# Kernel tuning notes

Hardware: AMD Instinct MI355X
Metric: run time of the kernel (lower is better)

Reference implementation:

```python
import jax, jax.numpy as jnp
import numpy as np

INPUT_SIZE = 64
HIDDEN = 256
BATCH = 128
SEQ = 1000


def setup_inputs() -> dict:
    key = jax.random.key(0)
    ks = jax.random.split(key, 17)
    s_in = 1.0 / np.sqrt(INPUT_SIZE)
    s_h = 1.0 / np.sqrt(HIDDEN)
    d = {"x": jax.random.normal(ks[0], (BATCH, SEQ, INPUT_SIZE), dtype=jnp.float32)}
    names_ih = ["W_ii", "W_if", "W_ig", "W_io"]
    names_hh = ["W_hi", "W_hf", "W_hg", "W_ho"]
    for i, n in enumerate(names_ih):
        d[n] = jax.random.uniform(ks[1 + i], (HIDDEN, INPUT_SIZE), minval=-s_in, maxval=s_in, dtype=jnp.float32)
        d["b" + n[1:]] = jax.random.uniform(ks[5 + i], (HIDDEN,), minval=-s_in, maxval=s_in, dtype=jnp.float32)
    for i, n in enumerate(names_hh):
        d[n] = jax.random.uniform(ks[9 + i], (HIDDEN, HIDDEN), minval=-s_h, maxval=s_h, dtype=jnp.float32)
        d["b" + n[1:]] = jax.random.uniform(ks[13 + i], (HIDDEN,), minval=-s_h, maxval=s_h, dtype=jnp.float32)
    return d


def _lstm(x, W_ii, b_ii, W_if, b_if, W_ig, b_ig, W_io, b_io,
          W_hi, b_hi, W_hf, b_hf, W_hg, b_hg, W_ho, b_ho):
    B = x.shape[0]
    H = W_ii.shape[0]
    # Precompute all input-to-hidden projections for every timestep in one
    # batched GEMM per gate (the recurrence only needs the h-to-h part).
    # Shapes: [B, T, H] each; then move time to the leading axis for scan.
    xi = jnp.einsum('bti,hi->tbh', x, W_ii) + b_ii
    xf = jnp.einsum('bti,hi->tbh', x, W_if) + b_if
    xg = jnp.einsum('bti,hi->tbh', x, W_ig) + b_ig
    xo = jnp.einsum('bti,hi->tbh', x, W_io) + b_io

    h0 = jnp.zeros((B, H), dtype=x.dtype)
    c0 = jnp.zeros((B, H), dtype=x.dtype)

    def step(carry, xs):
        h, c = carry
        xi_t, xf_t, xg_t, xo_t = xs
        i_t = jax.nn.sigmoid(xi_t + h @ W_hi.T + b_hi)
        f_t = jax.nn.sigmoid(xf_t + h @ W_hf.T + b_hf)
        g_t = jnp.tanh(xg_t + h @ W_hg.T + b_hg)
        o_t = jax.nn.sigmoid(xo_t + h @ W_ho.T + b_ho)
        c_new = f_t * c + i_t * g_t
        h_new = o_t * jnp.tanh(c_new)
        return (h_new, c_new), h_new

    (h_n, c_n), out_tbh = jax.lax.scan(step, (h0, c0), (xi, xf, xg, xo))
    output = jnp.transpose(out_tbh, (1, 0, 2))  # [B, T, H]
    return output, h_n[None], c_n[None]


def reference(x, W_ii, b_ii, W_if, b_if, W_ig, b_ig, W_io, b_io,
              W_hi, b_hi, W_hf, b_hf, W_hg, b_hg, W_ho, b_ho):
    return _lstm(x, W_ii, b_ii, W_if, b_if, W_ig, b_ig, W_io, b_io,
                 W_hi, b_hi, W_hf, b_hf, W_hg, b_hg, W_ho, b_ho)
```

## Files before the change

### kernel.cpp

```cpp
#include <hip/hip_runtime.h>

#define INPUT 64
#define HID 256
#define BATCH 128
#define TSTEPS 1000
#define KTOT 320

typedef __bf16 bf16_t;
typedef __bf16 bf16x8 __attribute__((ext_vector_type(8)));
typedef float  f32x4  __attribute__((ext_vector_type(4)));

#define WPACK_OFF   0
#define WPACK_BYTES (1024 * KTOT * 2)
#define BIAS_OFF    (WPACK_OFF + WPACK_BYTES)
#define BIAS_BYTES  (1024 * 4)
#define EXCH_OFF    (BIAS_OFF + BIAS_BYTES)
#define EXCH_BYTES  (16 * 2 * 2048 * 2)
#define FLAG_OFF    (EXCH_OFF + EXCH_BYTES)

__global__ void lstm_prep(
    const float* __restrict__ Wii, const float* __restrict__ Wif,
    const float* __restrict__ Wig, const float* __restrict__ Wio,
    const float* __restrict__ Whi, const float* __restrict__ Whf,
    const float* __restrict__ Whg, const float* __restrict__ Who,
    const float* __restrict__ bii, const float* __restrict__ bif,
    const float* __restrict__ big, const float* __restrict__ bio,
    const float* __restrict__ bhi, const float* __restrict__ bhf,
    const float* __restrict__ bhg, const float* __restrict__ bho,
    bf16_t* __restrict__ wpack, float* __restrict__ bias,
    int* __restrict__ flags)
{
    int id = blockIdx.x * 256 + threadIdx.x;
    if (id < 1024 * KTOT) {
        int n = id / KTOT, k = id % KTOT;
        int g = n >> 8, j = n & 255;
        const float* Wh = (g == 0) ? Whi : (g == 1) ? Whf : (g == 2) ? Whg : Who;
        const float* Wi = (g == 0) ? Wii : (g == 1) ? Wif : (g == 2) ? Wig : Wio;
        float v = (k < HID) ? Wh[j * HID + k] : Wi[j * INPUT + (k - HID)];
        wpack[id] = (bf16_t)v;
    }
    if (id < 1024) {
        int g = id >> 8, j = id & 255;
        const float* bi = (g == 0) ? bii : (g == 1) ? bif : (g == 2) ? big : bio;
        const float* bh = (g == 0) ? bhi : (g == 1) ? bhf : (g == 2) ? bhg : bho;
        bias[id] = bi[j] + bh[j];
    }
    if (id < 16)
        __hip_atomic_store(flags + id * 64, 0, __ATOMIC_RELAXED, __HIP_MEMORY_SCOPE_AGENT);
}

__device__ __forceinline__ float sigmoid_f(float v) {
    return 1.0f / (1.0f + __expf(-v));
}
__device__ __forceinline__ float tanh_f(float v) {
    return 1.0f - 2.0f / (__expf(2.0f * v) + 1.0f);
}

__global__ __launch_bounds__(512) void lstm_main(
    const float* __restrict__ x, const bf16_t* __restrict__ wpack,
    const float* __restrict__ bias_g, float* __restrict__ out,
    bf16_t* __restrict__ exch, int* __restrict__ flags)
{
    __shared__ __align__(16) bf16_t hxx[2][16 * 328];

    const int bid   = blockIdx.x;
    const int group = bid & 7;
    const int half  = bid >> 3;
    const int tid   = threadIdx.x;
    const int w     = tid >> 6;
    const int l     = tid & 63;
    const int col   = l & 15;
    const int kb    = l >> 4;

    const int jloc  = w * 16 + col;
    const int jglob = half * 128 + jloc;

    bf16x8 bW[4][10];
#pragma unroll
    for (int g = 0; g < 4; ++g) {
        const bf16_t* wrow = wpack + (size_t)(g * 256 + jglob) * KTOT;
#pragma unroll
        for (int ks = 0; ks < 10; ++ks)
            bW[g][ks] = *(const bf16x8*)(wrow + ks * 32 + kb * 8);
    }
#pragma unroll
    for (int g = 0; g < 4; ++g)
#pragma unroll
        for (int ks = 0; ks < 10; ++ks)
            asm volatile("" : "+v"(bW[g][ks]));

    float bias_r[4];
#pragma unroll
    for (int g = 0; g < 4; ++g)
        bias_r[g] = bias_g[g * 256 + jglob];

    float c_st[4] = {0.f, 0.f, 0.f, 0.f};

    const int pbid = (1 - half) * 8 + group;
    int*       flag_me = flags + bid * 64;
    const int* flag_pn = flags + pbid * 64;
    const int  pbase   = (1 - half) * 128;

    const int xb = tid >> 5;
    const int xi = (tid & 31) * 2;
    const float* xbase = x + (size_t)(group * 16 + xb) * (TSTEPS * INPUT) + xi;

    const int prow = tid >> 5;
    const int pe0  = (tid & 31) * 4;

    {
        float2 v = *(const float2*)(xbase);
        hxx[0][xb * 328 + 256 + xi]     = (bf16_t)v.x;
        hxx[0][xb * 328 + 256 + xi + 1] = (bf16_t)v.y;
    }
    float2 xv = *(const float2*)(xbase + INPUT);
    __syncthreads();

#pragma unroll 1
    for (int t = 0; t < TSTEPS; ++t) {
        const int cur = t & 1;
        const int nxt = cur ^ 1;

        if (t + 1 < TSTEPS) {
            hxx[nxt][xb * 328 + 256 + xi]     = (bf16_t)xv.x;
            hxx[nxt][xb * 328 + 256 + xi + 1] = (bf16_t)xv.y;
        }
        if (t + 2 < TSTEPS)
            xv = *(const float2*)(xbase + (size_t)(t + 2) * INPUT);
        if (t > 0) {
            if (l == 0) {
                while (__hip_atomic_load(flag_pn, __ATOMIC_RELAXED, __HIP_MEMORY_SCOPE_AGENT) < t) {}
            }
            const bf16_t* src = exch + ((size_t)pbid * 2 + ((t - 1) & 1)) * 2048
                              + prow * 128 + pe0;
            float2 v;
            asm volatile(
                "global_load_dwordx2 %0, %1, off sc0\n\t"
                "s_waitcnt vmcnt(0)"
                : "=&v"(v) : "v"(src) : "memory");
            *(float2*)&hxx[cur][prow * 328 + pbase + pe0] = v;
        }
        __syncthreads();

        f32x4 acc[4];
#pragma unroll
        for (int g = 0; g < 4; ++g)
            acc[g] = (f32x4){bias_r[g], bias_r[g], bias_r[g], bias_r[g]};

        const bf16_t* arow = &hxx[cur][col * 328 + kb * 8];
        {
            bf16x8 a8 = *(const bf16x8*)(arow + 8 * 32);
            bf16x8 a9 = *(const bf16x8*)(arow + 9 * 32);
#pragma unroll
            for (int g = 0; g < 4; ++g) {
                acc[g] = __builtin_amdgcn_mfma_f32_16x16x32_bf16(a8, bW[g][8], acc[g], 0, 0, 0);
                acc[g] = __builtin_amdgcn_mfma_f32_16x16x32_bf16(a9, bW[g][9], acc[g], 0, 0, 0);
            }
        }
        if (t > 0) {
#pragma unroll
            for (int ks = 0; ks < 8; ++ks) {
                bf16x8 a = *(const bf16x8*)(arow + ks * 32);
#pragma unroll
                for (int g = 0; g < 4; ++g)
                    acc[g] = __builtin_amdgcn_mfma_f32_16x16x32_bf16(a, bW[g][ks], acc[g], 0, 0, 0);
            }
        }

        bf16_t* pub = exch + ((size_t)bid * 2 + cur) * 2048;
        float hv[4];
#pragma unroll
        for (int r = 0; r < 4; ++r) {
            float gi = sigmoid_f(acc[0][r]);
            float gf = sigmoid_f(acc[1][r]);
            float gg = tanh_f(acc[2][r]);
            float go = sigmoid_f(acc[3][r]);
            float c  = gf * c_st[r] + gi * gg;
            c_st[r]  = c;
            float h  = go * tanh_f(c);
            hv[r]    = h;
            bf16_t hb = (bf16_t)h;
            const int row = kb * 4 + r;
            hxx[nxt][row * 328 + jglob] = hb;
            pub[row * 128 + jloc]       = hb;
        }
        __syncthreads();
        if (tid == 0)
            __hip_atomic_store(flag_me, t + 1, __ATOMIC_RELAXED, __HIP_MEMORY_SCOPE_AGENT);

#pragma unroll
        for (int r = 0; r < 4; ++r) {
            const int row = kb * 4 + r;
            const int bg  = group * 16 + row;
            out[((size_t)bg * TSTEPS + t) * HID + jglob] = hv[r];
        }
        if (t == TSTEPS - 1) {
            float* hn = out + (size_t)BATCH * TSTEPS * HID;
            float* cn = hn + (size_t)BATCH * HID;
#pragma unroll
            for (int r = 0; r < 4; ++r) {
                const int row = kb * 4 + r;
                const int bg  = group * 16 + row;
                hn[(size_t)bg * HID + jglob] = hv[r];
                cn[(size_t)bg * HID + jglob] = c_st[r];
            }
        }
    }
}

extern "C" void kernel_launch(void* const* d_in, const int* in_sizes, int n_in,
                              void* d_out, int out_size, void* d_ws, size_t ws_size,
                              hipStream_t stream)
{
    (void)in_sizes; (void)n_in; (void)out_size; (void)ws_size;
    const float* x   = (const float*)d_in[0];
    const float* Wii = (const float*)d_in[1];
    const float* bii = (const float*)d_in[2];
    const float* Wif = (const float*)d_in[3];
    const float* bif = (const float*)d_in[4];
    const float* Wig = (const float*)d_in[5];
    const float* big = (const float*)d_in[6];
    const float* Wio = (const float*)d_in[7];
    const float* bio = (const float*)d_in[8];
    const float* Whi = (const float*)d_in[9];
    const float* bhi = (const float*)d_in[10];
    const float* Whf = (const float*)d_in[11];
    const float* bhf = (const float*)d_in[12];
    const float* Whg = (const float*)d_in[13];
    const float* bhg = (const float*)d_in[14];
    const float* Who = (const float*)d_in[15];
    const float* bho = (const float*)d_in[16];

    char* ws = (char*)d_ws;
    bf16_t* wpack = (bf16_t*)(ws + WPACK_OFF);
    float*  bias  = (float*)(ws + BIAS_OFF);
    bf16_t* exch  = (bf16_t*)(ws + EXCH_OFF);
    int*    flags = (int*)(ws + FLAG_OFF);

    lstm_prep<<<(1024 * KTOT + 255) / 256, 256, 0, stream>>>(
        Wii, Wif, Wig, Wio, Whi, Whf, Whg, Who,
        bii, bif, big, bio, bhi, bhf, bhg, bho,
        wpack, bias, flags);

    lstm_main<<<16, 512, 0, stream>>>(
        x, wpack, bias, (float*)d_out, exch, flags);
}
```

Measured before the change: 2.626 ms.

## Halve threads per block, give each wave two column tiles of weights

Each block now runs 4 waves instead of 8, and each wave keeps weights for two 16-column tiles in registers, giving 80 bf16x8 register vectors. The partner exchange and x loads are widened to match the new thread count (dwordx4 and float4). The aim is to reduce per-step barrier cost and wave count while keeping MFMA work per block the same. In exchange, each wave issues twice as many MFMAs serially and register pressure rises sharply, so waves_per_eu is pinned to 1.

```diff
diff --git a/kernel.cpp b/kernel.cpp
--- a/kernel.cpp
+++ b/kernel.cpp
@@ -56,7 +56,8 @@
     return 1.0f - 2.0f / (__expf(2.0f * v) + 1.0f);
 }
 
-__global__ __launch_bounds__(512) void lstm_main(
+__global__ __launch_bounds__(256) __attribute__((amdgpu_waves_per_eu(1, 1)))
+void lstm_main(
     const float* __restrict__ x, const bf16_t* __restrict__ wpack,
     const float* __restrict__ bias_g, float* __restrict__ out,
     bf16_t* __restrict__ exch, int* __restrict__ flags)
@@ -71,49 +72,54 @@
     const int l     = tid & 63;
     const int col   = l & 15;
     const int kb    = l >> 4;
-
-    const int jloc  = w * 16 + col;
-    const int jglob = half * 128 + jloc;
-
-    bf16x8 bW[4][10];
-#pragma unroll
-    for (int g = 0; g < 4; ++g) {
-        const bf16_t* wrow = wpack + (size_t)(g * 256 + jglob) * KTOT;
-#pragma unroll
-        for (int ks = 0; ks < 10; ++ks)
-            bW[g][ks] = *(const bf16x8*)(wrow + ks * 32 + kb * 8);
-    }
+    const int jbase = w * 32;
+
+    bf16x8 bW[4][2][10];
 #pragma unroll
     for (int g = 0; g < 4; ++g)
 #pragma unroll
-        for (int ks = 0; ks < 10; ++ks)
-            asm volatile("" : "+v"(bW[g][ks]));
-
-    float bias_r[4];
+        for (int n = 0; n < 2; ++n) {
+            const int jg = half * 128 + jbase + n * 16 + col;
+            const bf16_t* wrow = wpack + (size_t)(g * 256 + jg) * KTOT;
+#pragma unroll
+            for (int ks = 0; ks < 10; ++ks)
+                bW[g][n][ks] = *(const bf16x8*)(wrow + ks * 32 + kb * 8);
+        }
 #pragma unroll
     for (int g = 0; g < 4; ++g)
-        bias_r[g] = bias_g[g * 256 + jglob];
-
-    float c_st[4] = {0.f, 0.f, 0.f, 0.f};
+#pragma unroll
+        for (int n = 0; n < 2; ++n)
+#pragma unroll
+            for (int ks = 0; ks < 10; ++ks)
+                asm volatile("" : "+v"(bW[g][n][ks]));
+
+    float bias_r[4][2];
+#pragma unroll
+    for (int g = 0; g < 4; ++g)
+#pragma unroll
+        for (int n = 0; n < 2; ++n)
+            bias_r[g][n] = bias_g[g * 256 + half * 128 + jbase + n * 16 + col];
+
+    float c_st[2][4] = {{0.f, 0.f, 0.f, 0.f}, {0.f, 0.f, 0.f, 0.f}};
 
     const int pbid = (1 - half) * 8 + group;
     int*       flag_me = flags + bid * 64;
     const int* flag_pn = flags + pbid * 64;
     const int  pbase   = (1 - half) * 128;
 
-    const int xb = tid >> 5;
-    const int xi = (tid & 31) * 2;
-    const float* xbase = x + (size_t)(group * 16 + xb) * (TSTEPS * INPUT) + xi;
-
-    const int prow = tid >> 5;
-    const int pe0  = (tid & 31) * 4;
+    const int prow = tid >> 4;
+    const int pe0  = (tid & 15) * 8;
+
+    const int xr  = tid >> 4;
+    const int xi0 = (tid & 15) * 4;
+    const float* xbase = x + (size_t)(group * 16 + xr) * (TSTEPS * INPUT) + xi0;
 
     {
-        float2 v = *(const float2*)(xbase);
-        hxx[0][xb * 328 + 256 + xi]     = (bf16_t)v.x;
-        hxx[0][xb * 328 + 256 + xi + 1] = (bf16_t)v.y;
-    }
-    float2 xv = *(const float2*)(xbase + INPUT);
+        float4 v = *(const float4*)(xbase);
+        bf16_t* d = &hxx[0][xr * 328 + 256 + xi0];
+        d[0] = (bf16_t)v.x; d[1] = (bf16_t)v.y; d[2] = (bf16_t)v.z; d[3] = (bf16_t)v.w;
+    }
+    float4 xv = *(const float4*)(xbase + INPUT);
     __syncthreads();
 
 #pragma unroll 1
@@ -122,40 +128,44 @@
         const int nxt = cur ^ 1;
 
         if (t + 1 < TSTEPS) {
-            hxx[nxt][xb * 328 + 256 + xi]     = (bf16_t)xv.x;
-            hxx[nxt][xb * 328 + 256 + xi + 1] = (bf16_t)xv.y;
+            bf16_t* d = &hxx[nxt][xr * 328 + 256 + xi0];
+            d[0] = (bf16_t)xv.x; d[1] = (bf16_t)xv.y; d[2] = (bf16_t)xv.z; d[3] = (bf16_t)xv.w;
         }
         if (t + 2 < TSTEPS)
-            xv = *(const float2*)(xbase + (size_t)(t + 2) * INPUT);
+            xv = *(const float4*)(xbase + (size_t)(t + 2) * INPUT);
         if (t > 0) {
             if (l == 0) {
                 while (__hip_atomic_load(flag_pn, __ATOMIC_RELAXED, __HIP_MEMORY_SCOPE_AGENT) < t) {}
             }
             const bf16_t* src = exch + ((size_t)pbid * 2 + ((t - 1) & 1)) * 2048
                               + prow * 128 + pe0;
-            float2 v;
+            f32x4 v0;
             asm volatile(
-                "global_load_dwordx2 %0, %1, off sc0\n\t"
+                "global_load_dwordx4 %0, %1, off sc0\n\t"
                 "s_waitcnt vmcnt(0)"
-                : "=&v"(v) : "v"(src) : "memory");
-            *(float2*)&hxx[cur][prow * 328 + pbase + pe0] = v;
+                : "=&v"(v0) : "v"(src) : "memory");
+            *(f32x4*)&hxx[cur][prow * 328 + pbase + pe0] = v0;
         }
         __syncthreads();
 
-        f32x4 acc[4];
+        f32x4 acc[4][2];
 #pragma unroll
         for (int g = 0; g < 4; ++g)
-            acc[g] = (f32x4){bias_r[g], bias_r[g], bias_r[g], bias_r[g]};
+#pragma unroll
+            for (int n = 0; n < 2; ++n)
+                acc[g][n] = (f32x4){bias_r[g][n], bias_r[g][n], bias_r[g][n], bias_r[g][n]};
 
         const bf16_t* arow = &hxx[cur][col * 328 + kb * 8];
         {
             bf16x8 a8 = *(const bf16x8*)(arow + 8 * 32);
             bf16x8 a9 = *(const bf16x8*)(arow + 9 * 32);
 #pragma unroll
-            for (int g = 0; g < 4; ++g) {
-                acc[g] = __builtin_amdgcn_mfma_f32_16x16x32_bf16(a8, bW[g][8], acc[g], 0, 0, 0);
-                acc[g] = __builtin_amdgcn_mfma_f32_16x16x32_bf16(a9, bW[g][9], acc[g], 0, 0, 0);
-            }
+            for (int g = 0; g < 4; ++g)
+#pragma unroll
+                for (int n = 0; n < 2; ++n) {
+                    acc[g][n] = __builtin_amdgcn_mfma_f32_16x16x32_bf16(a8, bW[g][n][8], acc[g][n], 0, 0, 0);
+                    acc[g][n] = __builtin_amdgcn_mfma_f32_16x16x32_bf16(a9, bW[g][n][9], acc[g][n], 0, 0, 0);
+                }
         }
         if (t > 0) {
 #pragma unroll
@@ -163,47 +173,58 @@
                 bf16x8 a = *(const bf16x8*)(arow + ks * 32);
 #pragma unroll
                 for (int g = 0; g < 4; ++g)
-                    acc[g] = __builtin_amdgcn_mfma_f32_16x16x32_bf16(a, bW[g][ks], acc[g], 0, 0, 0);
+#pragma unroll
+                    for (int n = 0; n < 2; ++n)
+                        acc[g][n] = __builtin_amdgcn_mfma_f32_16x16x32_bf16(a, bW[g][n][ks], acc[g][n], 0, 0, 0);
             }
         }
 
         bf16_t* pub = exch + ((size_t)bid * 2 + cur) * 2048;
-        float hv[4];
-#pragma unroll
-        for (int r = 0; r < 4; ++r) {
-            float gi = sigmoid_f(acc[0][r]);
-            float gf = sigmoid_f(acc[1][r]);
-            float gg = tanh_f(acc[2][r]);
-            float go = sigmoid_f(acc[3][r]);
-            float c  = gf * c_st[r] + gi * gg;
-            c_st[r]  = c;
-            float h  = go * tanh_f(c);
-            hv[r]    = h;
-            bf16_t hb = (bf16_t)h;
-            const int row = kb * 4 + r;
-            hxx[nxt][row * 328 + jglob] = hb;
-            pub[row * 128 + jloc]       = hb;
-        }
+        float hv[2][4];
+#pragma unroll
+        for (int n = 0; n < 2; ++n)
+#pragma unroll
+            for (int r = 0; r < 4; ++r) {
+                float gi = sigmoid_f(acc[0][n][r]);
+                float gf = sigmoid_f(acc[1][n][r]);
+                float gg = tanh_f(acc[2][n][r]);
+                float go = sigmoid_f(acc[3][n][r]);
+                float c  = gf * c_st[n][r] + gi * gg;
+                c_st[n][r] = c;
+                float h  = go * tanh_f(c);
+                hv[n][r] = h;
+                bf16_t hb = (bf16_t)h;
+                const int row = kb * 4 + r;
+                const int jl  = jbase + n * 16 + col;
+                hxx[nxt][row * 328 + half * 128 + jl] = hb;
+                pub[row * 128 + jl]                   = hb;
+            }
         __syncthreads();
         if (tid == 0)
             __hip_atomic_store(flag_me, t + 1, __ATOMIC_RELAXED, __HIP_MEMORY_SCOPE_AGENT);
 
 #pragma unroll
-        for (int r = 0; r < 4; ++r) {
-            const int row = kb * 4 + r;
-            const int bg  = group * 16 + row;
-            out[((size_t)bg * TSTEPS + t) * HID + jglob] = hv[r];
-        }
+        for (int n = 0; n < 2; ++n)
+#pragma unroll
+            for (int r = 0; r < 4; ++r) {
+                const int row = kb * 4 + r;
+                const int bg  = group * 16 + row;
+                const int jg  = half * 128 + jbase + n * 16 + col;
+                out[((size_t)bg * TSTEPS + t) * HID + jg] = hv[n][r];
+            }
         if (t == TSTEPS - 1) {
             float* hn = out + (size_t)BATCH * TSTEPS * HID;
             float* cn = hn + (size_t)BATCH * HID;
 #pragma unroll
-            for (int r = 0; r < 4; ++r) {
-                const int row = kb * 4 + r;
-                const int bg  = group * 16 + row;
-                hn[(size_t)bg * HID + jglob] = hv[r];
-                cn[(size_t)bg * HID + jglob] = c_st[r];
-            }
+            for (int n = 0; n < 2; ++n)
+#pragma unroll
+                for (int r = 0; r < 4; ++r) {
+                    const int row = kb * 4 + r;
+                    const int bg  = group * 16 + row;
+                    const int jg  = half * 128 + jbase + n * 16 + col;
+                    hn[(size_t)bg * HID + jg] = hv[n][r];
+                    cn[(size_t)bg * HID + jg] = c_st[n][r];
+                }
         }
     }
 }
@@ -242,6 +263,6 @@
         bii, bif, big, bio, bhi, bhf, bhg, bho,
         wpack, bias, flags);
 
-    lstm_main<<<16, 512, 0, stream>>>(
+    lstm_main<<<16, 256, 0, stream>>>(
         x, wpack, bias, (float*)d_out, exch, flags);
 }
```

Result: slower. 3.012 ms (+14.7%).
